# Optimization experiments

Measured on AMD Instinct MI355X. Metric: run time of the kernel, lower is better.

## Reference

```python
import jax, jax.numpy as jnp
import numpy as np

B, S, D, H = 2, 2048, 1024, 16
HD = D // H  # head_dim = 64

def setup_inputs() -> dict:
    key = jax.random.key(0)
    ks = jax.random.split(key, 6)
    sc = 0.02
    return {
        "x": jax.random.normal(ks[0], (B, S, D), dtype=jnp.float32),
        "Wq": jax.random.normal(ks[1], (D, D), dtype=jnp.float32) * sc,
        "Wk": jax.random.normal(ks[2], (D, D), dtype=jnp.float32) * sc,
        "Wv": jax.random.normal(ks[3], (D, D), dtype=jnp.float32) * sc,
        "Wo": jax.random.normal(ks[4], (D, D), dtype=jnp.float32) * sc,
        "bo": jnp.zeros((D,), dtype=jnp.float32),
    }

def reference(x, Wq, Wk, Wv, Wo, bo):
    b, s, d = x.shape
    # QKV projections (no bias, qkv_bias=False)
    q = (x @ Wq).reshape(b, s, H, HD).transpose(0, 2, 1, 3)  # [b,h,s,hd]
    k = (x @ Wk).reshape(b, s, H, HD).transpose(0, 2, 1, 3)
    v = (x @ Wv).reshape(b, s, H, HD).transpose(0, 2, 1, 3)
    scores = jnp.einsum("bhqd,bhkd->bhqk", q, k)  # [b,h,s,s]
    causal = jnp.triu(jnp.ones((s, s), dtype=bool), k=1)
    scores = jnp.where(causal, -jnp.inf, scores)
    # NOTE: source divides by keys.shape[-1]**0 / 5 == 1/5 -> scores / 5 (faithful)
    attn = jax.nn.softmax(scores / 5.0, axis=-1)
    ctx = jnp.einsum("bhqk,bhkd->bhqd", attn, v)  # [b,h,s,hd]
    ctx = ctx.transpose(0, 2, 1, 3).reshape(b, s, d)
    return ctx @ Wo + bo
```

## Files before the change

### kernel.cpp

```cpp
#include <hip/hip_runtime.h>
#include <math.h>

#define BB 2
#define SS 2048
#define DD 1024
#define HH 16
#define HD 64
#define MM (BB*SS)

typedef float  f32x4 __attribute__((ext_vector_type(4)));
typedef short  s16x8 __attribute__((ext_vector_type(8)));
typedef unsigned short u16;
typedef u16    u16x4 __attribute__((ext_vector_type(4)));
typedef unsigned int u32;
typedef u32    u32x2 __attribute__((ext_vector_type(2)));
typedef u32    u32x4 __attribute__((ext_vector_type(4)));

static __device__ __forceinline__ u16 f2bf(float f) {
    u32 u = __float_as_uint(f);
    u = (u + 0x7FFFu + ((u >> 16) & 1u)) >> 16;
    return (u16)u;
}

static __device__ __forceinline__ u32 cvtpk_bf16(float lo, float hi) {
    u32 r;
    asm("v_cvt_pk_bf16_f32 %0, %1, %2" : "=v"(r) : "v"(lo), "v"(hi));
    return r;
}

static __device__ __forceinline__ void gload16(const u16* g, void* l) {
    __builtin_amdgcn_global_load_lds((const __attribute__((address_space(1))) u32*)g,
                                     (__attribute__((address_space(3))) u32*)l, 16, 0, 0);
}

__global__ __launch_bounds__(256) void conv_x(const float* __restrict__ in,
                                              u16* __restrict__ outb) {
    int i = blockIdx.x * 256 + threadIdx.x;
    const f32x4* p = (const f32x4*)in;
    f32x4 a = p[i*2], b = p[i*2 + 1];
    u16x4 lo, hi;
    lo[0]=f2bf(a.x); lo[1]=f2bf(a.y); lo[2]=f2bf(a.z); lo[3]=f2bf(a.w);
    hi[0]=f2bf(b.x); hi[1]=f2bf(b.y); hi[2]=f2bf(b.z); hi[3]=f2bf(b.w);
    *(u16x4*)(outb + (size_t)i*8)     = lo;
    *(u16x4*)(outb + (size_t)i*8 + 4) = hi;
}

__global__ __launch_bounds__(256) void conv_wt(const float* __restrict__ W0,
                                               const float* __restrict__ W1,
                                               const float* __restrict__ W2,
                                               const float* __restrict__ W3,
                                               u16* __restrict__ WT) {
    const int z = blockIdx.z;
    const float* W = (z==0) ? W0 : (z==1) ? W1 : (z==2) ? W2 : W3;
    u16* dst = WT + (size_t)z * 1024 * 1024;
    __shared__ u16 tr[64][72];
    const int t = threadIdx.x;
    const int r0 = blockIdx.y * 64, c0 = blockIdx.x * 64;
    #pragma unroll
    for (int u = 0; u < 4; ++u) {
        int idx = u*256 + t;
        int r = idx >> 4, c4 = (idx & 15) * 4;
        f32x4 v = *(const f32x4*)(W + (size_t)(r0 + r)*1024 + c0 + c4);
        tr[c4+0][r] = f2bf(v.x);
        tr[c4+1][r] = f2bf(v.y);
        tr[c4+2][r] = f2bf(v.z);
        tr[c4+3][r] = f2bf(v.w);
    }
    __syncthreads();
    {
        int c = t >> 2, rq = (t & 3) * 16;
        u32x4 v0 = *(const u32x4*)&tr[c][rq];
        u32x4 v1 = *(const u32x4*)&tr[c][rq + 8];
        u16* op = dst + (size_t)(c0 + c)*1024 + r0 + rq;
        *(u32x4*)op       = v0;
        *(u32x4*)(op + 8) = v1;
    }
}

template<int EPI, int NJ>
__global__ __launch_bounds__(256) void mfma_gemm(const u16* __restrict__ A,
                                                 const u16* __restrict__ WT,
                                                 const float* __restrict__ bias,
                                                 u16* __restrict__ Qb,
                                                 u16* __restrict__ Kb,
                                                 u16* __restrict__ Vtb,
                                                 float* __restrict__ outF) {
    constexpr int BN  = NJ * 32;
    constexpr int ASZ = 16384;
    constexpr int BSZ = NJ * 4096;
    __shared__ u32x4 smemv[(2*(ASZ + BSZ))/16];
    char* smem = (char*)smemv;
    char* A0 = smem;
    char* B0 = smem + ASZ;
    char* A1 = smem + ASZ + BSZ;
    char* B1 = smem + 2*ASZ + BSZ;
    const int t   = threadIdx.x;
    const int w   = t >> 6;
    const int l   = t & 63;
    const int c15 = l & 15;
    const int g16 = ((l >> 4) & 3) << 4;
    const int mw  = w >> 1, nw = w & 1;
    const int brow = blockIdx.y * 128;
    const int bcol = blockIdx.x * BN;

    f32x4 acc[4][NJ] = {};

    const u16* Asrc = A  + (size_t)brow * DD;
    const u16* Bsrc = WT + (size_t)bcol * DD;

    auto stage = [&](int k0, char* Ab, char* Bb) {
        #pragma unroll
        for (int u = 0; u < 4; ++u) {
            int idx = u*256 + t;
            int row = idx >> 3;
            int cb  = (idx & 7) << 4;
            int off = (cb ^ ((row & 7) << 4)) >> 1;
            gload16(Asrc + (size_t)row*DD + k0 + off, Ab + ((idx - l) << 4));
        }
        #pragma unroll
        for (int u = 0; u < NJ; ++u) {
            int idx = u*256 + t;
            int row = idx >> 3;
            int cb  = (idx & 7) << 4;
            int off = (cb ^ ((row & 7) << 4)) >> 1;
            gload16(Bsrc + (size_t)row*DD + k0 + off, Bb + ((idx - l) << 4));
        }
    };

    auto compute = [&](char* Ab, char* Bb) {
        s16x8 af[4][2], bf[NJ][2];
        #pragma unroll
        for (int mi = 0; mi < 4; ++mi) {
            int row = mw*64 + mi*16 + c15;
            int sw  = (row & 7) << 4;
            af[mi][0] = *(const s16x8*)(Ab + row*128 + ((g16)      ^ sw));
            af[mi][1] = *(const s16x8*)(Ab + row*128 + ((64 + g16) ^ sw));
        }
        #pragma unroll
        for (int nj = 0; nj < NJ; ++nj) {
            int row = nw*(NJ*16) + nj*16 + c15;
            int sw  = (row & 7) << 4;
            bf[nj][0] = *(const s16x8*)(Bb + row*128 + ((g16)      ^ sw));
            bf[nj][1] = *(const s16x8*)(Bb + row*128 + ((64 + g16) ^ sw));
        }
        #pragma unroll
        for (int c = 0; c < 2; ++c)
            #pragma unroll
            for (int mi = 0; mi < 4; ++mi)
                #pragma unroll
                for (int nj = 0; nj < NJ; ++nj)
                    acc[mi][nj] = __builtin_amdgcn_mfma_f32_16x16x32_bf16(
                        af[mi][c], bf[nj][c], acc[mi][nj], 0, 0, 0);
    };

    stage(0, A0, B0);
    __syncthreads();
    for (int k0 = 0; k0 < DD; k0 += 128) {
        stage(k0 + 64, A1, B1);
        compute(A0, B0);
        __syncthreads();
        if (k0 + 128 < DD) stage(k0 + 128, A0, B0);
        compute(A1, B1);
        __syncthreads();
    }

    if constexpr (EPI == 1) {
        #pragma unroll
        for (int mi = 0; mi < 4; ++mi)
            #pragma unroll
            for (int r = 0; r < 4; ++r) {
                int mg = brow + mw*64 + mi*16 + ((l >> 4) & 3)*4 + r;
                #pragma unroll
                for (int nj = 0; nj < NJ; ++nj) {
                    int nc = bcol + nw*(NJ*16) + nj*16 + c15;
                    outF[(size_t)mg*DD + nc] = acc[mi][nj][r] + bias[nc];
                }
            }
    } else {
        const int wq   = blockIdx.x >> 3;
        const int ncw0 = (blockIdx.x & 7)*128 + nw*64;
        if (wq < 2) {
            u16* dst  = wq ? Kb : Qb;
            float scl = wq ? 1.0f : 0.28853900817779268f;
            #pragma unroll
            for (int mi = 0; mi < 4; ++mi)
                #pragma unroll
                for (int r = 0; r < 4; ++r) {
                    int mg = brow + mw*64 + mi*16 + ((l >> 4) & 3)*4 + r;
                    int b_ = mg >> 11, s_ = mg & (SS-1);
                    #pragma unroll
                    for (int nj = 0; nj < NJ; ++nj) {
                        int nc = ncw0 + nj*16 + c15;
                        int h_ = nc >> 6, d_ = nc & 63;
                        dst[(((size_t)b_*HH + h_)*SS + s_)*HD + d_] =
                            f2bf(acc[mi][nj][r] * scl);
                    }
                }
        } else {
            char* tw = smem + w*8192;
            #pragma unroll
            for (int nj = 0; nj < NJ; ++nj)
                #pragma unroll
                for (int mi = 0; mi < 4; ++mi)
                    #pragma unroll
                    for (int r = 0; r < 4; ++r) {
                        int n = nj*16 + c15;
                        int m = mi*16 + ((l >> 4) & 3)*4 + r;
                        *(u16*)(tw + n*128 + ((m*2) ^ ((n & 7) << 4))) =
                            f2bf(acc[mi][nj][r]);
                    }
            __syncthreads();
            #pragma unroll
            for (int it = 0; it < 8; ++it) {
                int n  = it*8 + (l >> 3);
                int mb = l & 7;
                u32x4 v = *(const u32x4*)(tw + n*128 + ((mb*16) ^ ((n & 7) << 4)));
                int nc = ncw0 + n;
                int h_ = nc >> 6, d_ = nc & 63;
                int mg0 = brow + mw*64;
                int b_ = mg0 >> 11;
                int sb = (mg0 & (SS-1)) + mb*8;
                *(u32x4*)(Vtb + (((size_t)b_*HH + h_)*HD + d_)*SS + sb) = v;
            }
        }
    }
}

__global__ __launch_bounds__(512) void attn_mfma(const u16* __restrict__ Q,
                                                 const u16* __restrict__ K,
                                                 const u16* __restrict__ Vt,
                                                 u16* __restrict__ ctx) {
    __shared__ u32x4 smemv[5120];
    char* smem = (char*)smemv;
    const int pr = blockIdx.x;
    const int h  = blockIdx.y;
    const int b  = blockIdx.z;
    const int t  = threadIdx.x;
    const int w  = t >> 6;
    const int l  = t & 63;
    const int g  = l >> 4;
    const int q15 = l & 15;
    char* Psm = smem + 65536 + w*2048;

    const size_t bh = ((size_t)b*HH + h) * SS;
    const u16* Kg = K  + bh * HD;
    const u16* Vg = Vt + ((size_t)(b*HH + h)) * HD * SS;

    #pragma unroll 1
    for (int half = 0; half < 2; ++half) {
        const int qb = half ? (15 - pr) : pr;
        const u16* Qw = Q + (bh + (size_t)qb*128 + w*16 + q15) * HD;
        s16x8 qf0 = *(const s16x8*)(Qw + g*8);
        s16x8 qf1 = *(const s16x8*)(Qw + 32 + g*8);

        f32x4 acc[4] = {};
        float lsum = 0.f;
        const int qg = qb*128 + w*16 + q15;

        u32x4 kreg[2], vreg[2];
        #pragma unroll
        for (int u = 0; u < 2; ++u) {
            int idx = u*512 + t;
            kreg[u] = *(const u32x4*)(Kg + (size_t)(idx >> 3)*HD + (idx & 7)*8);
            vreg[u] = *(const u32x4*)(Vg + (size_t)(idx >> 4)*SS + (idx & 15)*8);
        }
        if (half) __syncthreads();
        #pragma unroll
        for (int u = 0; u < 2; ++u) {
            int idx = u*512 + t;
            int kr = idx >> 3, kc = (idx & 7) << 4;
            *(u32x4*)(smem + kr*128 + (kc ^ ((kr & 7) << 4))) = kreg[u];
            int vr = idx >> 4, vc = (idx & 15) << 4;
            *(u32x4*)(smem + 32768 + vr*256 + (vc ^ ((vr & 7) << 4))) = vreg[u];
        }

        int cur = 0;
        for (int kt = 0; kt <= qb; ++kt) {
            const bool pf = (kt < qb);
            if (pf) {
                #pragma unroll
                for (int u = 0; u < 2; ++u) {
                    int idx = u*512 + t;
                    kreg[u] = *(const u32x4*)(Kg + (size_t)((kt+1)*128 + (idx >> 3))*HD + (idx & 7)*8);
                    vreg[u] = *(const u32x4*)(Vg + (size_t)(idx >> 4)*SS + (kt+1)*128 + (idx & 15)*8);
                }
            }
            __syncthreads();
            char* Kc = smem + (cur << 14);
            char* Vc = smem + 32768 + (cur << 14);

            f32x4 st[8];
            __builtin_amdgcn_s_setprio(1);
            #pragma unroll
            for (int kb = 0; kb < 8; ++kb) {
                f32x4 z = {0.f, 0.f, 0.f, 0.f};
                int row = kb*16 + q15;
                int sw  = (row & 7) << 4;
                s16x8 a0 = *(const s16x8*)(Kc + row*128 + ((g*16)      ^ sw));
                s16x8 a1 = *(const s16x8*)(Kc + row*128 + ((64 + g*16) ^ sw));
                z = __builtin_amdgcn_mfma_f32_16x16x32_bf16(a0, qf0, z, 0, 0, 0);
                z = __builtin_amdgcn_mfma_f32_16x16x32_bf16(a1, qf1, z, 0, 0, 0);
                st[kb] = z;
            }
            __builtin_amdgcn_s_setprio(0);

            if (kt == qb) {
                #pragma unroll
                for (int kb = 0; kb < 8; ++kb)
                    #pragma unroll
                    for (int r = 0; r < 4; ++r) {
                        int key = kt*128 + kb*16 + g*4 + r;
                        if (key > qg) st[kb][r] = -1e30f;
                    }
            }

            {
                float p0 = 0.f, p1 = 0.f, p2 = 0.f, p3 = 0.f;
                #pragma unroll
                for (int kb = 0; kb < 8; ++kb) {
                    float e0 = __builtin_amdgcn_exp2f(st[kb][0]);
                    float e1 = __builtin_amdgcn_exp2f(st[kb][1]);
                    float e2 = __builtin_amdgcn_exp2f(st[kb][2]);
                    float e3 = __builtin_amdgcn_exp2f(st[kb][3]);
                    st[kb][0] = e0; st[kb][1] = e1;
                    st[kb][2] = e2; st[kb][3] = e3;
                    p0 += e0; p1 += e1; p2 += e2; p3 += e3;
                }
                float ps = (p0 + p1) + (p2 + p3);
                ps += __shfl_xor(ps, 16);
                ps += __shfl_xor(ps, 32);
                lsum += ps;
            }

            {
                int swp = (q15 & 7) << 4;
                #pragma unroll
                for (int hf = 0; hf < 2; ++hf) {
                    #pragma unroll
                    for (int kb2 = 0; kb2 < 4; ++kb2) {
                        int kb = hf*4 + kb2;
                        u32x2 pk2;
                        pk2[0] = cvtpk_bf16(st[kb][0], st[kb][1]);
                        pk2[1] = cvtpk_bf16(st[kb][2], st[kb][3]);
                        *(u32x2*)(Psm + q15*128 + ((kb2*32 + g*8) ^ swp)) = pk2;
                    }
                    s16x8 pa[2];
                    #pragma unroll
                    for (int cl = 0; cl < 2; ++cl)
                        pa[cl] = *(const s16x8*)(Psm + q15*128 + ((cl*64 + g*16) ^ swp));
                    __builtin_amdgcn_s_setprio(1);
                    #pragma unroll
                    for (int n = 0; n < 4; ++n) {
                        int row = n*16 + q15;
                        int sw  = (row & 7) << 4;
                        #pragma unroll
                        for (int cl = 0; cl < 2; ++cl) {
                            int c = hf*2 + cl;
                            s16x8 vv = *(const s16x8*)(Vc + row*256 + ((c*64 + g*16) ^ sw));
                            acc[n] = __builtin_amdgcn_mfma_f32_16x16x32_bf16(pa[cl], vv, acc[n], 0, 0, 0);
                        }
                    }
                    __builtin_amdgcn_s_setprio(0);
                }
            }

            if (pf) {
                char* Kn = smem + ((cur ^ 1) << 14);
                char* Vn = smem + 32768 + ((cur ^ 1) << 14);
                #pragma unroll
                for (int u = 0; u < 2; ++u) {
                    int idx = u*512 + t;
                    int kr = idx >> 3, kc = (idx & 7) << 4;
                    *(u32x4*)(Kn + kr*128 + (kc ^ ((kr & 7) << 4))) = kreg[u];
                    int vr = idx >> 4, vc = (idx & 15) << 4;
                    *(u32x4*)(Vn + vr*256 + (vc ^ ((vr & 7) << 4))) = vreg[u];
                }
            }
            cur ^= 1;
        }

        #pragma unroll
        for (int r = 0; r < 4; ++r) {
            float inv = 1.f / __shfl(lsum, g*4 + r);
            int qrow = qb*128 + w*16 + g*4 + r;
            u16* crow = ctx + ((size_t)b*SS + qrow)*DD + h*HD;
            #pragma unroll
            for (int n = 0; n < 4; ++n)
                crow[n*16 + q15] = f2bf(acc[n][r] * inv);
        }
    }
}

extern "C" void kernel_launch(void* const* d_in, const int* in_sizes, int n_in,
                              void* d_out, int out_size, void* d_ws, size_t ws_size,
                              hipStream_t stream) {
    const float* x  = (const float*)d_in[0];
    const float* Wq = (const float*)d_in[1];
    const float* Wk = (const float*)d_in[2];
    const float* Wv = (const float*)d_in[3];
    const float* Wo = (const float*)d_in[4];
    const float* bo = (const float*)d_in[5];
    float* out = (float*)d_out;

    const size_t NELT = (size_t)MM * DD;
    const size_t NW   = (size_t)1024 * 1024;
    u16* wsb  = (u16*)d_ws;
    u16* xb   = wsb;
    u16* WT   = wsb + NELT;
    u16* Qb   = wsb + NELT + 4*NW;
    u16* Kb   = Qb + NELT;
    u16* Vtb  = Kb + NELT;
    u16* Ctxb = Vtb + NELT;
    u16* WTqkv = WT;
    u16* WTo   = WT + 3*NW;

    hipLaunchKernelGGL(conv_x, dim3(2048), dim3(256), 0, stream, x, xb);
    hipLaunchKernelGGL(conv_wt, dim3(16,16,4), dim3(256), 0, stream, Wq, Wk, Wv, Wo, WT);

    hipLaunchKernelGGL((mfma_gemm<0,4>), dim3(24,32), dim3(256), 0, stream,
                       xb, WTqkv, nullptr, Qb, Kb, Vtb, nullptr);

    hipLaunchKernelGGL(attn_mfma, dim3(8,16,2), dim3(512), 0, stream, Qb, Kb, Vtb, Ctxb);

    hipLaunchKernelGGL((mfma_gemm<1,2>), dim3(16,32), dim3(256), 0, stream,
                       Ctxb, WTo, bo, nullptr, nullptr, nullptr, out);
}
```

Measured before the change: 97.76 us.

## Split causal attention key range across two blocks with a combine pass

The attention grid doubles from 8 to 16 blocks per head. Each pair of query tiles is now split so one block handles the short tile plus the first half of the long tile's keys, and a second block handles the remaining keys of the long tile. The partial context and row sums of the long tile are merged by a new combine kernel that weights the two bf16 partials by their softmax sums. This gives 512 equal-sized blocks instead of 256, aiming to fill more CUs. The cost is an extra launch, extra global traffic for the partials, and extra bf16 rounding of intermediates.

```diff
diff --git a/kernel.cpp b/kernel.cpp
--- a/kernel.cpp
+++ b/kernel.cpp
@@ -20,6 +20,9 @@
     u32 u = __float_as_uint(f);
     u = (u + 0x7FFFu + ((u >> 16) & 1u)) >> 16;
     return (u16)u;
+}
+static __device__ __forceinline__ float bf2f(u16 v) {
+    return __uint_as_float(((u32)v) << 16);
 }
 
 static __device__ __forceinline__ u32 cvtpk_bf16(float lo, float hi) {
@@ -229,10 +232,15 @@
 __global__ __launch_bounds__(512) void attn_mfma(const u16* __restrict__ Q,
                                                  const u16* __restrict__ K,
                                                  const u16* __restrict__ Vt,
-                                                 u16* __restrict__ ctx) {
+                                                 u16* __restrict__ ctx,
+                                                 u16* __restrict__ P1,
+                                                 float* __restrict__ L0,
+                                                 float* __restrict__ L1) {
     __shared__ u32x4 smemv[5120];
     char* smem = (char*)smemv;
-    const int pr = blockIdx.x;
+    const int sp = blockIdx.x;
+    const int pr = sp >> 1;
+    const int side = sp & 1;
     const int h  = blockIdx.y;
     const int b  = blockIdx.z;
     const int t  = threadIdx.x;
@@ -245,10 +253,10 @@
     const size_t bh = ((size_t)b*HH + h) * SS;
     const u16* Kg = K  + bh * HD;
     const u16* Vg = Vt + ((size_t)(b*HH + h)) * HD * SS;
-
-    #pragma unroll 1
-    for (int half = 0; half < 2; ++half) {
-        const int qb = half ? (15 - pr) : pr;
+    const int pidx = (b*HH + h)*8 + pr;
+
+    auto segment = [&](int qb, int kt0, int ktlast, bool maskLast, int wmode,
+                       bool syncBefore) {
         const u16* Qw = Q + (bh + (size_t)qb*128 + w*16 + q15) * HD;
         s16x8 qf0 = *(const s16x8*)(Qw + g*8);
         s16x8 qf1 = *(const s16x8*)(Qw + 32 + g*8);
@@ -261,10 +269,10 @@
         #pragma unroll
         for (int u = 0; u < 2; ++u) {
             int idx = u*512 + t;
-            kreg[u] = *(const u32x4*)(Kg + (size_t)(idx >> 3)*HD + (idx & 7)*8);
-            vreg[u] = *(const u32x4*)(Vg + (size_t)(idx >> 4)*SS + (idx & 15)*8);
-        }
-        if (half) __syncthreads();
+            kreg[u] = *(const u32x4*)(Kg + (size_t)(kt0*128 + (idx >> 3))*HD + (idx & 7)*8);
+            vreg[u] = *(const u32x4*)(Vg + (size_t)(idx >> 4)*SS + kt0*128 + (idx & 15)*8);
+        }
+        if (syncBefore) __syncthreads();
         #pragma unroll
         for (int u = 0; u < 2; ++u) {
             int idx = u*512 + t;
@@ -275,8 +283,8 @@
         }
 
         int cur = 0;
-        for (int kt = 0; kt <= qb; ++kt) {
-            const bool pf = (kt < qb);
+        for (int kt = kt0; kt <= ktlast; ++kt) {
+            const bool pf = (kt < ktlast);
             if (pf) {
                 #pragma unroll
                 for (int u = 0; u < 2; ++u) {
@@ -304,7 +312,7 @@
             }
             __builtin_amdgcn_s_setprio(0);
 
-            if (kt == qb) {
+            if (maskLast && kt == ktlast) {
                 #pragma unroll
                 for (int kb = 0; kb < 8; ++kb)
                     #pragma unroll
@@ -383,12 +391,58 @@
         for (int r = 0; r < 4; ++r) {
             float inv = 1.f / __shfl(lsum, g*4 + r);
             int qrow = qb*128 + w*16 + g*4 + r;
-            u16* crow = ctx + ((size_t)b*SS + qrow)*DD + h*HD;
-            #pragma unroll
-            for (int n = 0; n < 4; ++n)
-                crow[n*16 + q15] = f2bf(acc[n][r] * inv);
-        }
-    }
+            if (wmode <= 1) {
+                u16* crow = ctx + ((size_t)b*SS + qrow)*DD + h*HD;
+                #pragma unroll
+                for (int n = 0; n < 4; ++n)
+                    crow[n*16 + q15] = f2bf(acc[n][r] * inv);
+            } else {
+                u16* prow = P1 + ((size_t)pidx*128 + (qrow - qb*128))*64;
+                #pragma unroll
+                for (int n = 0; n < 4; ++n)
+                    prow[n*16 + q15] = f2bf(acc[n][r] * inv);
+            }
+        }
+        if (wmode == 1 && l < 16) L0[pidx*128 + w*16 + q15] = lsum;
+        if (wmode == 2 && l < 16) L1[pidx*128 + w*16 + q15] = lsum;
+    };
+
+    if (side == 0) {
+        segment(pr,      0,      pr,      true,  0, false);
+        segment(15 - pr, 0,      7 - pr,  false, 1, true);
+    } else {
+        segment(15 - pr, 8 - pr, 15 - pr, true,  2, false);
+    }
+}
+
+__global__ __launch_bounds__(256) void combine_ctx(u16* __restrict__ ctx,
+                                                   const u16* __restrict__ P1,
+                                                   const float* __restrict__ L0,
+                                                   const float* __restrict__ L1) {
+    int idx = blockIdx.x * 256 + threadIdx.x;
+    int rg  = idx >> 3;
+    int d8  = (idx & 7) * 8;
+    int pidx = rg >> 7;
+    int row  = rg & 127;
+    int b  = pidx >> 7;
+    int hh = (pidx >> 3) & 15;
+    int pr = pidx & 7;
+    int qb = 15 - pr;
+    float l0 = L0[rg], l1 = L1[rg];
+    float inv = 1.f / (l0 + l1);
+    float w0 = l0 * inv, w1 = l1 * inv;
+    u16* crow = ctx + ((size_t)b*SS + qb*128 + row)*DD + hh*HD + d8;
+    const u16* prow = P1 + ((size_t)rg)*64 + d8;
+    u16x4 c0a = *(u16x4*)crow, c0b = *(u16x4*)(crow + 4);
+    u16x4 c1a = *(const u16x4*)prow, c1b = *(const u16x4*)(prow + 4);
+    u16x4 oa, ob;
+    #pragma unroll
+    for (int j = 0; j < 4; ++j) {
+        oa[j] = f2bf(bf2f(c0a[j])*w0 + bf2f(c1a[j])*w1);
+        ob[j] = f2bf(bf2f(c0b[j])*w0 + bf2f(c1b[j])*w1);
+    }
+    *(u16x4*)crow       = oa;
+    *(u16x4*)(crow + 4) = ob;
 }
 
 extern "C" void kernel_launch(void* const* d_in, const int* in_sizes, int n_in,
@@ -411,6 +465,9 @@
     u16* Kb   = Qb + NELT;
     u16* Vtb  = Kb + NELT;
     u16* Ctxb = Vtb + NELT;
+    u16* P1b  = Ctxb + NELT;
+    float* L0b = (float*)(P1b + (size_t)2*1024*1024);
+    float* L1b = L0b + 32768;
     u16* WTqkv = WT;
     u16* WTo   = WT + 3*NW;
 
@@ -420,7 +477,10 @@
     hipLaunchKernelGGL((mfma_gemm<0,4>), dim3(24,32), dim3(256), 0, stream,
                        xb, WTqkv, nullptr, Qb, Kb, Vtb, nullptr);
 
-    hipLaunchKernelGGL(attn_mfma, dim3(8,16,2), dim3(512), 0, stream, Qb, Kb, Vtb, Ctxb);
+    hipLaunchKernelGGL(attn_mfma, dim3(16,16,2), dim3(512), 0, stream,
+                       Qb, Kb, Vtb, Ctxb, P1b, L0b, L1b);
+    hipLaunchKernelGGL(combine_ctx, dim3(1024), dim3(256), 0, stream,
+                       Ctxb, P1b, L0b, L1b);
 
     hipLaunchKernelGGL((mfma_gemm<1,2>), dim3(16,32), dim3(256), 0, stream,
                        Ctxb, WTo, bo, nullptr, nullptr, nullptr, out);
```

New measurement: 104.3 us. 6.7% more time.
